# Optimization experiments

Hardware: AMD Instinct MI355X
Metric: run time of the kernel (lower is better)

## Reference

```python
import jax, jax.numpy as jnp
import numpy as np

EPS = 1e-08

def setup_inputs() -> dict:
    key = jax.random.key(0)
    k1, k2, k3 = jax.random.split(key, 3)
    b, cin, cout, ksz, h, w = 16, 256, 256, 3, 64, 64
    return {
        "x": jax.random.normal(k1, (b, cin, h, w), dtype=jnp.float32),
        "s": jax.random.normal(k2, (b, cin), dtype=jnp.float32),
        "weight": jax.random.normal(k3, (cout, cin, ksz, ksz), dtype=jnp.float32),
    }

def reference(x, s, weight):
    # x: [b, cin, h, w]; s: [b, cin]; weight: [cout, cin, k, k]
    b, cin, h, w = x.shape
    cout, _, ksz, _ = weight.shape
    pad = ksz // 2
    # demodulate pre-normalization of weight and style
    wn = weight * jax.lax.rsqrt(jnp.mean(jnp.square(weight), axis=(1, 2, 3), keepdims=True))
    sn = s * jax.lax.rsqrt(jnp.mean(jnp.square(s)))
    # per-sample modulation: [b, cout, cin, k, k]
    wmod = wn[None, :, :, :, :] * sn[:, None, :, None, None]
    # demodulation: normalize each output filter per sample
    sigma_inv = jax.lax.rsqrt(jnp.sum(jnp.square(wmod), axis=(2, 3, 4), keepdims=True) + EPS)
    wmod = wmod * sigma_inv
    # batch-grouped conv: input [1, b*cin, h, w], weight [b*cout, cin, k, k]
    xg = x.reshape(1, b * cin, h, w)
    wg = wmod.reshape(b * cout, cin, ksz, ksz)
    y = jax.lax.conv_general_dilated(
        xg, wg,
        window_strides=(1, 1),
        padding=[(pad, pad), (pad, pad)],
        feature_group_count=b,
        dimension_numbers=("NCHW", "OIHW", "NCHW"),
    )
    return y.reshape(b, cout, h, w)
```

## Files before the change

### kernel.cpp

```cpp
#include <hip/hip_runtime.h>
#include <hip/hip_bf16.h>

#define EPS 1e-8f
#define B_  16
#define CIN 256
#define COUT 256
#define HW 64

typedef __bf16 bf16x8 __attribute__((ext_vector_type(8)));
typedef float  f32x4  __attribute__((ext_vector_type(4)));

__device__ __forceinline__ void async16(void* lds, const void* g) {
    __builtin_amdgcn_global_load_lds(
        (const __attribute__((address_space(1))) unsigned int*)g,
        (__attribute__((address_space(3))) unsigned int*)lds,
        16, 0, 0);
}

__global__ __launch_bounds__(256) void stats_kernel(const float* __restrict__ w,
                                                    const float* __restrict__ s,
                                                    float* __restrict__ wsq,
                                                    float* __restrict__ wn_scale,
                                                    float* __restrict__ ssum_out) {
    __shared__ float smem[4];
    const int t = threadIdx.x;
    const int lane = t & 63, wid = t >> 6;
    if (blockIdx.x == 256) {
        float v = 0.f;
        for (int i = t; i < B_ * CIN; i += 256) { float sv = s[i]; v += sv * sv; }
        for (int off = 32; off > 0; off >>= 1) v += __shfl_down(v, off, 64);
        if (lane == 0) smem[wid] = v;
        __syncthreads();
        if (t == 0) ssum_out[0] = smem[0] + smem[1] + smem[2] + smem[3];
        return;
    }
    const int co = blockIdx.x;
    const float* wp = w + ((size_t)co * CIN + t) * 9;
    float q = 0.f;
#pragma unroll
    for (int tp = 0; tp < 9; ++tp) { float wv = wp[tp]; q += wv * wv; }
    wsq[co * CIN + t] = q;
    float v = q;
    for (int off = 32; off > 0; off >>= 1) v += __shfl_down(v, off, 64);
    if (lane == 0) smem[wid] = v;
    __syncthreads();
    if (t == 0) wn_scale[co] = rsqrtf((smem[0] + smem[1] + smem[2] + smem[3]) / 2304.f);
}

__global__ __launch_bounds__(256) void wmod_kernel(const float* __restrict__ w,
                                                   const float* __restrict__ s,
                                                   const float* __restrict__ wsq,
                                                   const float* __restrict__ wn_scale,
                                                   const float* __restrict__ ssum,
                                                   __bf16* __restrict__ wfull) {
    __shared__ float smem[4];
    __shared__ float coef_s;
    const int co = blockIdx.x;
    const int b  = blockIdx.y;
    const int ci = threadIdx.x;
    const int lane = ci & 63, wid = ci >> 6;
    const float sv = s[b * CIN + ci];
    float v = sv * sv * wsq[co * CIN + ci];
    for (int off = 32; off > 0; off >>= 1) v += __shfl_down(v, off, 64);
    if (lane == 0) smem[wid] = v;
    __syncthreads();
    if (ci == 0) {
        float S = smem[0] + smem[1] + smem[2] + smem[3];
        float sn2 = (float)(B_ * CIN) / ssum[0];
        float wn = wn_scale[co];
        coef_s = wn * sqrtf(sn2) * rsqrtf(wn * wn * sn2 * S + EPS);
    }
    __syncthreads();
    const float sc = sv * coef_s;
    const float* wp = w + ((size_t)co * CIN + ci) * 9;
    float wv[9];
#pragma unroll
    for (int tp = 0; tp < 9; ++tp) wv[tp] = wp[tp];
    const size_t obase = ((size_t)b * 9) * 65536 + (size_t)(ci >> 5) * 8192
                       + (size_t)co * 32 + (ci & 31);
#pragma unroll
    for (int tap = 0; tap < 9; ++tap)
        wfull[obase + (size_t)tap * 65536] = (__bf16)(wv[tap] * sc);
}

__device__ __forceinline__ uint pack2(float lo, float hi) {
    __bf16 a = (__bf16)lo, b = (__bf16)hi;
    unsigned short ua = __builtin_bit_cast(unsigned short, a);
    unsigned short ub = __builtin_bit_cast(unsigned short, b);
    return ((uint)ub << 16) | (uint)ua;
}

__global__ __launch_bounds__(256) void xbf2_kernel(const float* __restrict__ x,
                                                   __bf16* __restrict__ xbf) {
    __shared__ uint xsd[64 * 160];
    const int row = blockIdx.x;
    const int b   = blockIdx.y;
    const int t   = threadIdx.x;
    const float* xbase = x + ((size_t)b * CIN * HW + row) * HW;
#pragma unroll
    for (int k = 0; k < 8; ++k) {
        int p   = k * 256 + t;
        int ci2 = p >> 4;
        int c4  = (p & 15) * 4;
        const float* src = xbase + (size_t)(2 * ci2) * (HW * HW) + c4;
        float4 v0 = *(const float4*)src;
        float4 v1 = *(const float4*)(src + HW * HW);
        const int dj = ci2 + (ci2 >> 2);
#pragma unroll
        for (int i = 0; i < 4; ++i)
            xsd[(c4 + i) * 160 + dj] = pack2((&v0.x)[i], (&v1.x)[i]);
    }
    __syncthreads();
    __bf16* orow = xbf + (((size_t)b * HW + row) * 64) * CIN;
#pragma unroll
    for (int k = 0; k < 8; ++k) {
        int o   = k * 256 + t;
        int col = o >> 5;
        int u   = o & 31;
        const uint* rp = &xsd[col * 160 + 5 * u];
        uint a0 = rp[0], a1 = rp[1], a2 = rp[2], a3 = rp[3];
        uint4 vv; vv.x = a0; vv.y = a1; vv.z = a2; vv.w = a3;
        *(uint4*)&orow[(size_t)col * CIN + u * 8] = vv;
    }
}

__global__ __launch_bounds__(256, 3) void conv_mfma3(const __bf16* __restrict__ xbf,
                                                     const __bf16* __restrict__ zrow,
                                                     const __bf16* __restrict__ wfull,
                                                     float* __restrict__ out) {
    __shared__ __attribute__((aligned(16))) __bf16 xs[2][800 * 8];

    const int bid = blockIdx.x;
    const int b    = (bid & 7) + ((bid >= 512) ? 8 : 0);
    const int row0 = (bid >> 3) & 63;
    const int t = threadIdx.x;
    const int wy = t >> 6, lane = t & 63;
    const int m16 = lane & 15, q = lane >> 4;

    const __bf16* gsrc[4];
    unsigned ldsoff[4];
    bool val[4];
#pragma unroll
    for (int i = 0; i < 4; ++i) {
        int slot = i * 256 + t;
        val[i] = slot < 800;
        int qq  = slot / 200;
        int rem = slot - qq * 200;
        int irow = rem / 66;
        int col  = rem - irow * 66;
        int gr = row0 - 1 + irow;
        const __bf16* g;
        if (!val[i] || rem >= 198) {
            g = zrow;
        } else if ((unsigned)gr < 64u && col != 0 && col != 65) {
            g = xbf + (((size_t)b * HW + gr) * 64 + (col - 1)) * CIN + qq * 8;
        } else {
            g = zrow + col * CIN + qq * 8;
        }
        gsrc[i] = g;
        ldsoff[i] = (unsigned)slot * 16;
    }

#pragma unroll
    for (int i = 0; i < 4; ++i)
        if (val[i]) async16((char*)xs[0] + ldsoff[i], gsrc[i]);

    f32x4 acc[4][4] = {};
    const __bf16* abase = wfull + (size_t)b * 589824
                        + (size_t)(wy * 64 + m16) * 32 + q * 8;

    bf16x8 afc[4], bfc[4];
#pragma unroll
    for (int i = 0; i < 4; ++i)
        afc[i] = *(const bf16x8*)(abase + i * 512);

    for (int cc = 0; cc < 8; ++cc) {
        const __bf16* wb = abase + (size_t)cc * 8192;
        __syncthreads();
        if (cc < 7) {
#pragma unroll
            for (int i = 0; i < 4; ++i)
                if (val[i]) async16((char*)xs[(cc + 1) & 1] + ldsoff[i], gsrc[i] + cc * 32 + 32);
        }
        const __bf16* xcur = xs[cc & 1];
        {
            const int rb = (q * 200 + m16) * 8;
#pragma unroll
            for (int j = 0; j < 4; ++j)
                bfc[j] = *(const bf16x8*)&xcur[rb + j * 128];
        }
#pragma unroll
        for (int tap = 0; tap < 9; ++tap) {
            bf16x8 afn[4], bfn[4];
            if (tap < 8) {
#pragma unroll
                for (int i = 0; i < 4; ++i)
                    afn[i] = *(const bf16x8*)(wb + (size_t)(tap + 1) * 65536 + i * 512);
                const int dr = (tap + 1) / 3, dc = (tap + 1) % 3;
                const int rb = (q * 200 + dr * 66 + m16 + dc) * 8;
#pragma unroll
                for (int j = 0; j < 4; ++j)
                    bfn[j] = *(const bf16x8*)&xcur[rb + j * 128];
            } else if (cc < 7) {
#pragma unroll
                for (int i = 0; i < 4; ++i)
                    afn[i] = *(const bf16x8*)(wb + 8192 + i * 512);
            }
            __builtin_amdgcn_s_setprio(1);
#pragma unroll
            for (int i = 0; i < 4; ++i)
#pragma unroll
                for (int j = 0; j < 4; ++j)
                    acc[i][j] = __builtin_amdgcn_mfma_f32_16x16x32_bf16(afc[i], bfc[j], acc[i][j], 0, 0, 0);
            __builtin_amdgcn_s_setprio(0);
            if (tap < 8) {
#pragma unroll
                for (int i = 0; i < 4; ++i) afc[i] = afn[i];
#pragma unroll
                for (int j = 0; j < 4; ++j) bfc[j] = bfn[j];
            } else if (cc < 7) {
#pragma unroll
                for (int i = 0; i < 4; ++i) afc[i] = afn[i];
            }
        }
    }

#pragma unroll
    for (int i = 0; i < 4; ++i) {
        const int cobase = wy * 64 + i * 16 + q * 4;
#pragma unroll
        for (int reg = 0; reg < 4; ++reg) {
            float* op = out + ((size_t)b * COUT + (cobase + reg)) * (HW * HW) + row0 * HW;
#pragma unroll
            for (int j = 0; j < 4; ++j)
                op[j * 16 + m16] = acc[i][j][reg];
        }
    }
}

extern "C" void kernel_launch(void* const* d_in, const int* in_sizes, int n_in,
                              void* d_out, int out_size, void* d_ws, size_t ws_size,
                              hipStream_t stream) {
    const float* x = (const float*)d_in[0];
    const float* s = (const float*)d_in[1];
    const float* w = (const float*)d_in[2];
    float* out = (float*)d_out;

    float* ws = (float*)d_ws;
    float*  ssum     = ws;
    float*  wn_scale = ws + 16;
    float*  wsq      = ws + 512;
    __bf16* wfull    = (__bf16*)(ws + 70656);
    __bf16* zrow     = (__bf16*)(ws + 4789248);
    __bf16* xbf      = (__bf16*)(ws + 4798464);

    hipMemsetAsync(zrow, 0, 36864, stream);
    stats_kernel<<<257, 256, 0, stream>>>(w, s, wsq, wn_scale, ssum);
    wmod_kernel<<<dim3(COUT, B_), 256, 0, stream>>>(w, s, wsq, wn_scale, ssum, wfull);
    xbf2_kernel<<<dim3(64, B_), 256, 0, stream>>>(x, xbf);
    conv_mfma3<<<1024, 256, 0, stream>>>(xbf, zrow, wfull, out);
}
```

Before: 217.7 us.

## Fuse preprocessing kernels into one launch and swizzle conv LDS layout

```diff
diff --git a/kernel.cpp b/kernel.cpp
--- a/kernel.cpp
+++ b/kernel.cpp
@@ -17,72 +17,6 @@
         16, 0, 0);
 }
 
-__global__ __launch_bounds__(256) void stats_kernel(const float* __restrict__ w,
-                                                    const float* __restrict__ s,
-                                                    float* __restrict__ wsq,
-                                                    float* __restrict__ wn_scale,
-                                                    float* __restrict__ ssum_out) {
-    __shared__ float smem[4];
-    const int t = threadIdx.x;
-    const int lane = t & 63, wid = t >> 6;
-    if (blockIdx.x == 256) {
-        float v = 0.f;
-        for (int i = t; i < B_ * CIN; i += 256) { float sv = s[i]; v += sv * sv; }
-        for (int off = 32; off > 0; off >>= 1) v += __shfl_down(v, off, 64);
-        if (lane == 0) smem[wid] = v;
-        __syncthreads();
-        if (t == 0) ssum_out[0] = smem[0] + smem[1] + smem[2] + smem[3];
-        return;
-    }
-    const int co = blockIdx.x;
-    const float* wp = w + ((size_t)co * CIN + t) * 9;
-    float q = 0.f;
-#pragma unroll
-    for (int tp = 0; tp < 9; ++tp) { float wv = wp[tp]; q += wv * wv; }
-    wsq[co * CIN + t] = q;
-    float v = q;
-    for (int off = 32; off > 0; off >>= 1) v += __shfl_down(v, off, 64);
-    if (lane == 0) smem[wid] = v;
-    __syncthreads();
-    if (t == 0) wn_scale[co] = rsqrtf((smem[0] + smem[1] + smem[2] + smem[3]) / 2304.f);
-}
-
-__global__ __launch_bounds__(256) void wmod_kernel(const float* __restrict__ w,
-                                                   const float* __restrict__ s,
-                                                   const float* __restrict__ wsq,
-                                                   const float* __restrict__ wn_scale,
-                                                   const float* __restrict__ ssum,
-                                                   __bf16* __restrict__ wfull) {
-    __shared__ float smem[4];
-    __shared__ float coef_s;
-    const int co = blockIdx.x;
-    const int b  = blockIdx.y;
-    const int ci = threadIdx.x;
-    const int lane = ci & 63, wid = ci >> 6;
-    const float sv = s[b * CIN + ci];
-    float v = sv * sv * wsq[co * CIN + ci];
-    for (int off = 32; off > 0; off >>= 1) v += __shfl_down(v, off, 64);
-    if (lane == 0) smem[wid] = v;
-    __syncthreads();
-    if (ci == 0) {
-        float S = smem[0] + smem[1] + smem[2] + smem[3];
-        float sn2 = (float)(B_ * CIN) / ssum[0];
-        float wn = wn_scale[co];
-        coef_s = wn * sqrtf(sn2) * rsqrtf(wn * wn * sn2 * S + EPS);
-    }
-    __syncthreads();
-    const float sc = sv * coef_s;
-    const float* wp = w + ((size_t)co * CIN + ci) * 9;
-    float wv[9];
-#pragma unroll
-    for (int tp = 0; tp < 9; ++tp) wv[tp] = wp[tp];
-    const size_t obase = ((size_t)b * 9) * 65536 + (size_t)(ci >> 5) * 8192
-                       + (size_t)co * 32 + (ci & 31);
-#pragma unroll
-    for (int tap = 0; tap < 9; ++tap)
-        wfull[obase + (size_t)tap * 65536] = (__bf16)(wv[tap] * sc);
-}
-
 __device__ __forceinline__ uint pack2(float lo, float hi) {
     __bf16 a = (__bf16)lo, b = (__bf16)hi;
     unsigned short ua = __builtin_bit_cast(unsigned short, a);
@@ -90,12 +24,73 @@
     return ((uint)ub << 16) | (uint)ua;
 }
 
-__global__ __launch_bounds__(256) void xbf2_kernel(const float* __restrict__ x,
-                                                   __bf16* __restrict__ xbf) {
+__global__ __launch_bounds__(256) void prep_kernel(const float* __restrict__ x,
+                                                   const float* __restrict__ s,
+                                                   const float* __restrict__ w,
+                                                   __bf16* __restrict__ xbf,
+                                                   __bf16* __restrict__ wfull,
+                                                   __bf16* __restrict__ zrow) {
     __shared__ uint xsd[64 * 160];
-    const int row = blockIdx.x;
-    const int b   = blockIdx.y;
+    __shared__ float red[8];
+    const int bid = blockIdx.x;
     const int t   = threadIdx.x;
+
+    if (bid == 256) {
+        uint4 z = make_uint4(0, 0, 0, 0);
+        uint4* zp = (uint4*)zrow;
+#pragma unroll
+        for (int k = 0; k < 9; ++k) zp[k * 256 + t] = z;
+        return;
+    }
+
+    if (bid < 256) {
+        const int co = bid;
+        const int ci = t;
+        const int lane = t & 63, wid = t >> 6;
+        float as = 0.f;
+#pragma unroll
+        for (int k = 0; k < 16; ++k) { float sv = s[k * 256 + t]; as += sv * sv; }
+        const float* wp = w + ((size_t)co * CIN + ci) * 9;
+        float wv[9];
+        float q = 0.f;
+#pragma unroll
+        for (int tp = 0; tp < 9; ++tp) { wv[tp] = wp[tp]; q += wv[tp] * wv[tp]; }
+        float a = as, qq = q;
+        for (int off = 32; off > 0; off >>= 1) {
+            a  += __shfl_down(a,  off, 64);
+            qq += __shfl_down(qq, off, 64);
+        }
+        if (lane == 0) { red[wid] = a; red[4 + wid] = qq; }
+        __syncthreads();
+        const float ssum = red[0] + red[1] + red[2] + red[3];
+        const float Sw   = red[4] + red[5] + red[6] + red[7];
+        const float sn2  = (float)(B_ * CIN) / ssum;
+        const float wn   = rsqrtf(Sw / 2304.f);
+        const float wn2sn2 = wn * wn * sn2;
+        const float wsn  = wn * sqrtf(sn2);
+
+        for (int b = 0; b < B_; ++b) {
+            const float sv = s[b * CIN + ci];
+            float v = sv * sv * q;
+            for (int off = 32; off > 0; off >>= 1) v += __shfl_down(v, off, 64);
+            __syncthreads();
+            if (lane == 0) red[wid] = v;
+            __syncthreads();
+            const float S = red[0] + red[1] + red[2] + red[3];
+            const float coef = wsn * rsqrtf(wn2sn2 * S + EPS);
+            const float sc = sv * coef;
+            const size_t obase = ((size_t)b * 9) * 65536 + (size_t)(ci >> 5) * 8192
+                               + (size_t)co * 32 + (ci & 31);
+#pragma unroll
+            for (int tap = 0; tap < 9; ++tap)
+                wfull[obase + (size_t)tap * 65536] = (__bf16)(wv[tap] * sc);
+        }
+        return;
+    }
+
+    const int idx = bid - 257;
+    const int row = idx & 63;
+    const int b   = idx >> 6;
     const float* xbase = x + ((size_t)b * CIN * HW + row) * HW;
 #pragma unroll
     for (int k = 0; k < 8; ++k) {
@@ -118,8 +113,7 @@
         int col = o >> 5;
         int u   = o & 31;
         const uint* rp = &xsd[col * 160 + 5 * u];
-        uint a0 = rp[0], a1 = rp[1], a2 = rp[2], a3 = rp[3];
-        uint4 vv; vv.x = a0; vv.y = a1; vv.z = a2; vv.w = a3;
+        uint4 vv; vv.x = rp[0]; vv.y = rp[1]; vv.z = rp[2]; vv.w = rp[3];
         *(uint4*)&orow[(size_t)col * CIN + u * 8] = vv;
     }
 }
@@ -128,7 +122,7 @@
                                                      const __bf16* __restrict__ zrow,
                                                      const __bf16* __restrict__ wfull,
                                                      float* __restrict__ out) {
-    __shared__ __attribute__((aligned(16))) __bf16 xs[2][800 * 8];
+    __shared__ __attribute__((aligned(16))) __bf16 xs[2][1024 * 8];
 
     const int bid = blockIdx.x;
     const int b    = (bid & 7) + ((bid >= 512) ? 8 : 0);
@@ -136,34 +130,29 @@
     const int t = threadIdx.x;
     const int wy = t >> 6, lane = t & 63;
     const int m16 = lane & 15, q = lane >> 4;
+    const int qx = q << 8;
 
     const __bf16* gsrc[4];
-    unsigned ldsoff[4];
-    bool val[4];
 #pragma unroll
     for (int i = 0; i < 4; ++i) {
-        int slot = i * 256 + t;
-        val[i] = slot < 800;
-        int qq  = slot / 200;
-        int rem = slot - qq * 200;
+        int rem  = t ^ i;
         int irow = rem / 66;
         int col  = rem - irow * 66;
-        int gr = row0 - 1 + irow;
+        int gr   = row0 - 1 + irow;
         const __bf16* g;
-        if (!val[i] || rem >= 198) {
+        if (rem >= 198) {
             g = zrow;
         } else if ((unsigned)gr < 64u && col != 0 && col != 65) {
-            g = xbf + (((size_t)b * HW + gr) * 64 + (col - 1)) * CIN + qq * 8;
+            g = xbf + (((size_t)b * HW + gr) * 64 + (col - 1)) * CIN + i * 8;
         } else {
-            g = zrow + col * CIN + qq * 8;
+            g = zrow + col * CIN + i * 8;
         }
         gsrc[i] = g;
-        ldsoff[i] = (unsigned)slot * 16;
     }
 
 #pragma unroll
     for (int i = 0; i < 4; ++i)
-        if (val[i]) async16((char*)xs[0] + ldsoff[i], gsrc[i]);
+        async16((char*)xs[0] + (i * 256 + t) * 16, gsrc[i]);
 
     f32x4 acc[4][4] = {};
     const __bf16* abase = wfull + (size_t)b * 589824
@@ -180,14 +169,15 @@
         if (cc < 7) {
 #pragma unroll
             for (int i = 0; i < 4; ++i)
-                if (val[i]) async16((char*)xs[(cc + 1) & 1] + ldsoff[i], gsrc[i] + cc * 32 + 32);
+                async16((char*)xs[(cc + 1) & 1] + (i * 256 + t) * 16, gsrc[i] + cc * 32 + 32);
         }
         const __bf16* xcur = xs[cc & 1];
         {
-            const int rb = (q * 200 + m16) * 8;
-#pragma unroll
-            for (int j = 0; j < 4; ++j)
-                bfc[j] = *(const bf16x8*)&xcur[rb + j * 128];
+#pragma unroll
+            for (int j = 0; j < 4; ++j) {
+                int phys = qx + ((m16 + j * 16) ^ q);
+                bfc[j] = *(const bf16x8*)&xcur[phys * 8];
+            }
         }
 #pragma unroll
         for (int tap = 0; tap < 9; ++tap) {
@@ -197,10 +187,12 @@
                 for (int i = 0; i < 4; ++i)
                     afn[i] = *(const bf16x8*)(wb + (size_t)(tap + 1) * 65536 + i * 512);
                 const int dr = (tap + 1) / 3, dc = (tap + 1) % 3;
-                const int rb = (q * 200 + dr * 66 + m16 + dc) * 8;
-#pragma unroll
-                for (int j = 0; j < 4; ++j)
-                    bfn[j] = *(const bf16x8*)&xcur[rb + j * 128];
+                const int rembase = dr * 66 + m16 + dc;
+#pragma unroll
+                for (int j = 0; j < 4; ++j) {
+                    int phys = qx + ((rembase + j * 16) ^ q);
+                    bfn[j] = *(const bf16x8*)&xcur[phys * 8];
+                }
             } else if (cc < 7) {
 #pragma unroll
                 for (int i = 0; i < 4; ++i)
@@ -247,16 +239,10 @@
     float* out = (float*)d_out;
 
     float* ws = (float*)d_ws;
-    float*  ssum     = ws;
-    float*  wn_scale = ws + 16;
-    float*  wsq      = ws + 512;
-    __bf16* wfull    = (__bf16*)(ws + 70656);
-    __bf16* zrow     = (__bf16*)(ws + 4789248);
-    __bf16* xbf      = (__bf16*)(ws + 4798464);
-
-    hipMemsetAsync(zrow, 0, 36864, stream);
-    stats_kernel<<<257, 256, 0, stream>>>(w, s, wsq, wn_scale, ssum);
-    wmod_kernel<<<dim3(COUT, B_), 256, 0, stream>>>(w, s, wsq, wn_scale, ssum, wfull);
-    xbf2_kernel<<<dim3(64, B_), 256, 0, stream>>>(x, xbf);
+    __bf16* wfull = (__bf16*)(ws + 70656);
+    __bf16* zrow  = (__bf16*)(ws + 4789248);
+    __bf16* xbf   = (__bf16*)(ws + 4798464);
+
+    prep_kernel<<<1281, 256, 0, stream>>>(x, s, w, xbf, wfull, zrow);
     conv_mfma3<<<1024, 256, 0, stream>>>(xbf, zrow, wfull, out);
 }
```

Result: slower. 247.3 us (+13.6%).
